# Performance work log

Hardware: AMD Instinct MI355X
Metric: run time of the kernel (lower is better)

The kernel has to match this reference:

```python
import jax, jax.numpy as jnp
import numpy as np

B, S, DIN = 2, 2048, 1024
H = 16
DK = 1024   # dim_key_query_all
DV = 1024   # dim_value_all
DOUT = 1024
HEAD_SIZE = DK / H  # attention_head_size (float division in source)
LN_EPS = 1e-5


def setup_inputs() -> dict:
    key = jax.random.key(0)
    ks = jax.random.split(key, 12)
    s_in = 1.0 / np.sqrt(DIN)
    s_dv = 1.0 / np.sqrt(DV)
    return {
        "hidden_states": jax.random.normal(ks[0], (B, S, DIN), jnp.float32),
        "Wq": jax.random.uniform(ks[1], (DK, DIN), jnp.float32, -s_in, s_in),
        "Wk": jax.random.uniform(ks[2], (DK, DIN), jnp.float32, -s_in, s_in),
        "Wcb": jax.random.uniform(ks[3], (H, DIN), jnp.float32, -s_in, s_in),
        "Wv": jax.random.uniform(ks[4], (DV, DIN), jnp.float32, -s_in, s_in),
        "bv": jax.random.uniform(ks[5], (DV,), jnp.float32, -s_in, s_in),
        "mixing": 0.2 * jax.random.normal(ks[6], (H, DK), jnp.float32),
        "Wd": jax.random.uniform(ks[7], (DOUT, DV), jnp.float32, -s_dv, s_dv),
        "bd": jax.random.uniform(ks[8], (DOUT,), jnp.float32, -s_dv, s_dv),
        "gamma": jnp.ones((DV,), jnp.float32),
        "beta": jnp.zeros((DV,), jnp.float32),
    }


def reference(hidden_states, Wq, Wk, Wcb, Wv, bv, mixing, Wd, bd, gamma, beta):
    x = hidden_states  # [B, S, DIN]; self-attention: from == to
    q = jnp.einsum('bsd,kd->bsk', x, Wq)  # [B,S,DK]
    k = jnp.einsum('bsd,kd->bsk', x, Wk)  # [B,S,DK]
    # scores[b,h,i,j] = sum_c q[b,i,c]*mixing[h,c]*k[b,j,c]
    scores = jnp.einsum('bic,hc,bjc->bhij', q, mixing, k)
    cb = jnp.einsum('bjd,hd->bhj', x, Wcb)  # content bias [B,H,S]
    scores = scores + cb[:, :, None, :]
    scores = scores / jnp.sqrt(jnp.asarray(HEAD_SIZE, scores.dtype))
    probs = jax.nn.softmax(scores, axis=-1)  # dropout p=0.0 -> identity
    v = jnp.einsum('bsd,vd->bsv', x, Wv) + bv  # [B,S,DV]
    v = v.reshape(B, S, H, DV // H)
    ctx = jnp.einsum('bhij,bjhv->bihv', probs, v).reshape(B, S, DV)
    out = jnp.einsum('bsv,ov->bso', ctx, Wd) + bd
    res = x + out
    mu = jnp.mean(res, axis=-1, keepdims=True)
    var = jnp.var(res, axis=-1, keepdims=True)
    out = (res - mu) * jax.lax.rsqrt(var + LN_EPS) * gamma + beta
    return (out,)
```

## Files before the change

kernel.cpp:

```cpp
#include <hip/hip_runtime.h>
#include <cstddef>
#include <cstdint>

#define B_    2
#define S_    2048
#define DIN_  1024
#define H_    16
#define DK_   1024
#define DV_   1024
#define DH_   64
#define DOUT_ 1024
#define M_    (B_ * S_)

typedef __attribute__((ext_vector_type(8)))  short short8;
typedef __attribute__((ext_vector_type(4)))  float float4v;
typedef __attribute__((ext_vector_type(16))) float float16v;
typedef _Float16 half8v __attribute__((ext_vector_type(8)));

__device__ __forceinline__ float bf16s_to_f(short s) {
  union { unsigned int u; float f; } cv;
  cv.u = ((unsigned int)(unsigned short)s) << 16;
  return cv.f;
}
__device__ __forceinline__ short f_to_bf16s(float f) {
  union { float f; unsigned int u; } cv;
  cv.f = f;
  unsigned int u = cv.u + 0x7FFFu + ((cv.u >> 16) & 1u);
  return (short)(u >> 16);
}
__device__ __forceinline__ short f_to_f16s(float f) {
  union { _Float16 h; short s; } cv;
  cv.h = (_Float16)f;
  return cv.s;
}
__device__ __forceinline__ unsigned pkrtz_u32(float a, float b) {
  union { __fp16 __attribute__((ext_vector_type(2))) h2; unsigned u; } cv;
  cv.h2 = __builtin_amdgcn_cvt_pkrtz(a, b);
  return cv.u;
}
__device__ __forceinline__ void gll16(const void* g, void* l) {
  __builtin_amdgcn_global_load_lds(
      (const __attribute__((address_space(1))) unsigned int*)g,
      (__attribute__((address_space(3))) unsigned int*)l, 16, 0, 0);
}

__global__ __launch_bounds__(256) void cast_kernel(const float* __restrict__ in,
                                                   short* __restrict__ out, int n4) {
  int i = blockIdx.x * 256 + threadIdx.x;
  if (i >= n4) return;
  float4 v = ((const float4*)in)[i];
  union { ushort4 u; short s[4]; } o;
  o.s[0] = f_to_bf16s(v.x); o.s[1] = f_to_bf16s(v.y);
  o.s[2] = f_to_bf16s(v.z); o.s[3] = f_to_bf16s(v.w);
  ((ushort4*)out)[i] = o.u;
}

__global__ __launch_bounds__(256) void cb_kernel(const float* __restrict__ x,
                                                 const float* __restrict__ Wcb,
                                                 float* __restrict__ CBs) {
  __shared__ float xs[DIN_];
  const int row = blockIdx.x;
  const int tid = threadIdx.x;
  #pragma unroll
  for (int it = 0; it < 4; ++it)
    xs[tid + it * 256] = x[(size_t)row * DIN_ + tid + it * 256];
  __syncthreads();
  const int lane = tid & 63, w = tid >> 6;
  const float SC = 0.125f * 1.44269504088896f;
  #pragma unroll
  for (int hh = 0; hh < 4; ++hh) {
    const int hidx = w * 4 + hh;
    float p = 0.f;
    for (int c = lane; c < DIN_; c += 64)
      p += xs[c] * Wcb[(size_t)hidx * DIN_ + c];
    #pragma unroll
    for (int mk = 1; mk < 64; mk <<= 1) p += __shfl_xor(p, mk);
    if (lane == 0) {
      const int bb = row / S_, ss = row % S_;
      CBs[((size_t)bb * H_ + hidx) * S_ + ss] = p * SC;
    }
  }
}

__global__ __launch_bounds__(256, 4) void gemm_nt(
    const short* __restrict__ A, const short* __restrict__ Bw,
    const float* __restrict__ bias, const float* __restrict__ resid,
    short* __restrict__ outb, float* __restrict__ outf, int mode) {
  const int KD = 1024, ND = 1024;
  __shared__ __align__(16) short As[64 * 128];
  __shared__ __align__(16) short Bs[64 * 128];
  const int tid  = threadIdx.x;
  const int lane = tid & 63;
  const int w    = tid >> 6;
  const int quad = lane >> 4;
  const int l16  = lane & 15;
  const int m0   = blockIdx.y * 64;
  const int n0   = blockIdx.x * 64;
  const int wm   = (w >> 1) * 32;
  const int wn   = (w & 1) * 32;

  const int drow = lane >> 4;
  const int dp   = lane & 15;

  const float4v zero = {0.f, 0.f, 0.f, 0.f};
  float4v acc[2][2];
  acc[0][0] = zero; acc[0][1] = zero; acc[1][0] = zero; acc[1][1] = zero;

  for (int k0 = 0; k0 < KD; k0 += 128) {
    __syncthreads();
    #pragma unroll
    for (int cc = 0; cc < 4; ++cc) {
      const int n = w * 4 + cc;
      const int r = 4 * n + drow;
      const int l = dp ^ (r & 15);
      gll16(A  + (size_t)(m0 + r) * KD + k0 + l * 8, &As[n * 512]);
      gll16(Bw + (size_t)(n0 + r) * KD + k0 + l * 8, &Bs[n * 512]);
    }
    __syncthreads();
    #pragma unroll
    for (int ks = 0; ks < 4; ++ks) {
      const int ca = ((ks * 4 + quad) ^ l16) * 8;
      short8 af0 = *(short8*)&As[(wm + l16) * 128 + ca];
      short8 af1 = *(short8*)&As[(wm + 16 + l16) * 128 + ca];
      short8 bg0 = *(short8*)&Bs[(wn + l16) * 128 + ca];
      short8 bg1 = *(short8*)&Bs[(wn + 16 + l16) * 128 + ca];
      acc[0][0] = __builtin_amdgcn_mfma_f32_16x16x32_bf16(af0, bg0, acc[0][0], 0, 0, 0);
      acc[0][1] = __builtin_amdgcn_mfma_f32_16x16x32_bf16(af0, bg1, acc[0][1], 0, 0, 0);
      acc[1][0] = __builtin_amdgcn_mfma_f32_16x16x32_bf16(af1, bg0, acc[1][0], 0, 0, 0);
      acc[1][1] = __builtin_amdgcn_mfma_f32_16x16x32_bf16(af1, bg1, acc[1][1], 0, 0, 0);
    }
  }

  #pragma unroll
  for (int mt = 0; mt < 2; ++mt)
    #pragma unroll
    for (int nt = 0; nt < 2; ++nt)
      #pragma unroll
      for (int r = 0; r < 4; ++r) {
        int row = m0 + wm + mt * 16 + quad * 4 + r;
        int col = n0 + wn + nt * 16 + l16;
        float v = acc[mt][nt][r];
        if (mode == 1 || mode == 5) v += bias[col];
        if (mode == 2)
          outf[(size_t)row * ND + col] = v + bias[col] + resid[(size_t)row * ND + col];
        else if (mode == 5) {
          int bb = row >> 11, ss = row & 2047;
          outb[((size_t)bb * DV_ + col) * S_ + ss] = f_to_f16s(v);
        } else if (mode == 4)
          outb[(size_t)row * ND + col] = f_to_f16s(v);
        else
          outb[(size_t)row * ND + col] = f_to_bf16s(v);
      }
}

__global__ __launch_bounds__(256, 2) void attn_kernel(
    const short* __restrict__ Qf, const short* __restrict__ Kf,
    const short* __restrict__ Vtf, const float* __restrict__ mixing,
    const float* __restrict__ CBs, short* __restrict__ ctxb) {
  __shared__ __align__(16) short KsF[2 * 128 * 64];
  __shared__ __align__(16) short Vt[64][136];
  __shared__ __align__(16) short mix_s[DK_];
  __shared__ float cb_s[128];

  const int tid  = threadIdx.x;
  const int lane = tid & 63;
  const int l32  = lane & 31;
  const int l1   = lane >> 5;
  const int w    = tid >> 6;

  const int F    = blockIdx.x;
  const int xcd  = F & 7, rest = F >> 3;
  const int b    = xcd >> 2;
  const int h    = (xcd & 3) * 4 + (rest & 3);
  const int i0   = (rest >> 2) * 128;

  const float SC = 0.125f * 1.44269504088896f;
  for (int c = tid; c < DK_; c += 256) {
    union { _Float16 h; short s; } cv;
    cv.h = (_Float16)(mixing[(size_t)h * DK_ + c] * SC);
    mix_s[c] = cv.s;
  }

  const int iq = i0 + w * 32 + l32;
  const short* qptr  = Qf + ((size_t)b * S_ + iq) * DK_;
  const short* kbase = Kf + (size_t)b * S_ * DK_;
  const short* vtb   = Vtf + ((size_t)b * DV_ + h * DH_) * S_;
  const float* cbp   = CBs + ((size_t)b * H_ + h) * S_;

  float16v accS[4], accO[2];
  #pragma unroll
  for (int g = 0; g < 2; ++g)
    #pragma unroll
    for (int r = 0; r < 16; ++r) accO[g][r] = 0.f;
  float m_run = -1e30f, l_run = 0.f;

  const int nrow = lane >> 3;
  const int dp8  = lane & 7;

  const int vrow = tid >> 2;
  const int vseg = (tid & 3) * 32;

  for (int j0 = 0; j0 < S_; j0 += 128) {
    short8 vreg[4];
    #pragma unroll
    for (int c = 0; c < 4; ++c)
      vreg[c] = *(const short8*)(vtb + (size_t)vrow * S_ + j0 + vseg + c * 8);
    float cbv = 0.f;
    if (tid < 128) cbv = cbp[j0 + tid];
    __syncthreads();
    #pragma unroll
    for (int c = 0; c < 4; ++c)
      *(short8*)&Vt[vrow][vseg + c * 8] = vreg[c];
    if (tid < 128) cb_s[tid] = cbv;

    #pragma unroll
    for (int cc = 0; cc < 4; ++cc) {
      const int n = w * 4 + cc;
      const int r = 8 * n + nrow;
      const int lchunk = dp8 ^ (r & 7);
      gll16(kbase + (size_t)(j0 + r) * DK_ + lchunk * 8, &KsF[n * 512]);
    }
    half8v qcur[4], qnext[4];
    #pragma unroll
    for (int ks = 0; ks < 4; ++ks) {
      qcur[ks] = *(const half8v*)(qptr + ks * 16 + l1 * 8);
      qnext[ks] = qcur[ks];
    }

    #pragma unroll
    for (int f = 0; f < 4; ++f)
      #pragma unroll
      for (int r = 0; r < 16; ++r) accS[f][r] = 0.f;

    __syncthreads();

    for (int t = 0; t < 16; ++t) {
      if (t < 15) {
        const int nb = (t + 1) & 1;
        #pragma unroll
        for (int cc = 0; cc < 4; ++cc) {
          const int n = w * 4 + cc;
          const int r = 8 * n + nrow;
          const int lchunk = dp8 ^ (r & 7);
          gll16(kbase + (size_t)(j0 + r) * DK_ + (t + 1) * 64 + lchunk * 8,
                &KsF[nb * 8192 + n * 512]);
        }
        #pragma unroll
        for (int ks = 0; ks < 4; ++ks)
          qnext[ks] = *(const half8v*)(qptr + (t + 1) * 64 + ks * 16 + l1 * 8);
      }
      const short* kb = &KsF[(t & 1) * 8192];
      __builtin_amdgcn_s_setprio(1);
      #pragma unroll
      for (int ks = 0; ks < 4; ++ks) {
        half8v mf = *(half8v*)&mix_s[t * 64 + ks * 16 + l1 * 8];
        half8v qm = qcur[ks] * mf;
        const int poff = (((2 * ks + l1) ^ (l32 & 7)) * 8) + l32 * 64;
        #pragma unroll
        for (int f = 0; f < 4; ++f) {
          half8v af = *(half8v*)&kb[f * 2048 + poff];
          accS[f] = __builtin_amdgcn_mfma_f32_32x32x16_f16(af, qm, accS[f], 0, 0, 0);
        }
      }
      __builtin_amdgcn_s_setprio(0);
      #pragma unroll
      for (int ks = 0; ks < 4; ++ks) qcur[ks] = qnext[ks];
      __syncthreads();
    }

    float tmax = -1e30f;
    #pragma unroll
    for (int f = 0; f < 4; ++f)
      #pragma unroll
      for (int q = 0; q < 4; ++q) {
        float4 cbq = *(float4*)&cb_s[f * 32 + q * 8 + l1 * 4];
        #pragma unroll
        for (int c = 0; c < 4; ++c) {
          accS[f][4 * q + c] += ((const float*)&cbq)[c];
          tmax = fmaxf(tmax, accS[f][4 * q + c]);
        }
      }
    tmax = fmaxf(tmax, __shfl_xor(tmax, 32));
    const float mnew = fmaxf(m_run, tmax);
    const float alpha = exp2f(m_run - mnew);
    float tsum = 0.f;
    #pragma unroll
    for (int f = 0; f < 4; ++f)
      #pragma unroll
      for (int r = 0; r < 16; ++r) {
        float pv = exp2f(accS[f][r] - mnew);
        accS[f][r] = pv;
        tsum += pv;
      }
    tsum += __shfl_xor(tsum, 32);
    l_run = l_run * alpha + tsum;
    m_run = mnew;
    #pragma unroll
    for (int g = 0; g < 2; ++g)
      #pragma unroll
      for (int r = 0; r < 16; ++r) accO[g][r] *= alpha;

    #pragma unroll
    for (int cpv = 0; cpv < 8; ++cpv) {
      const int t = cpv & 1, fp = cpv >> 1;
      float xo[4], yo[4], lo[4], hi[4];
      #pragma unroll
      for (int c = 0; c < 4; ++c) {
        xo[c] = __shfl_xor(accS[fp][8 * t + c], 32);
        yo[c] = __shfl_xor(accS[fp][8 * t + 4 + c], 32);
      }
      #pragma unroll
      for (int c = 0; c < 4; ++c) {
        lo[c] = l1 ? yo[c] : accS[fp][8 * t + c];
        hi[c] = l1 ? accS[fp][8 * t + 4 + c] : xo[c];
      }
      union { half8v v; unsigned u[4]; } pb;
      pb.u[0] = pkrtz_u32(lo[0], lo[1]);
      pb.u[1] = pkrtz_u32(lo[2], lo[3]);
      pb.u[2] = pkrtz_u32(hi[0], hi[1]);
      pb.u[3] = pkrtz_u32(hi[2], hi[3]);
      #pragma unroll
      for (int g = 0; g < 2; ++g) {
        half8v vf = *(half8v*)&Vt[g * 32 + l32][cpv * 16 + l1 * 8];
        accO[g] = __builtin_amdgcn_mfma_f32_32x32x16_f16(vf, pb.v, accO[g], 0, 0, 0);
      }
    }
  }

  const float rl = 1.0f / l_run;
  short* cbase = ctxb + ((size_t)b * S_ + iq) * DV_ + h * DH_;
  #pragma unroll
  for (int g = 0; g < 2; ++g)
    #pragma unroll
    for (int q = 0; q < 4; ++q) {
      const int dv = g * 32 + 8 * q + 4 * l1;
      union { ushort4 u4; short s[4]; } ov;
      #pragma unroll
      for (int r = 0; r < 4; ++r)
        ov.s[r] = f_to_bf16s(accO[g][4 * q + r] * rl);
      *(ushort4*)(cbase + dv) = ov.u4;
    }
}

__global__ __launch_bounds__(256) void ln_kernel(float* __restrict__ out,
                                                 const float* __restrict__ gamma,
                                                 const float* __restrict__ beta) {
  __shared__ float red[8];
  const int row = blockIdx.x;
  const int tid = threadIdx.x;
  float* p = out + (size_t)row * DOUT_;
  float4 v = ((const float4*)p)[tid];
  float s = v.x + v.y + v.z + v.w;
  #pragma unroll
  for (int mk = 1; mk < 64; mk <<= 1) s += __shfl_xor(s, mk);
  if ((tid & 63) == 0) red[tid >> 6] = s;
  __syncthreads();
  const float mean = (red[0] + red[1] + red[2] + red[3]) * (1.0f / 1024.0f);
  const float d0 = v.x - mean, d1 = v.y - mean, d2 = v.z - mean, d3 = v.w - mean;
  float sq = d0 * d0 + d1 * d1 + d2 * d2 + d3 * d3;
  #pragma unroll
  for (int mk = 1; mk < 64; mk <<= 1) sq += __shfl_xor(sq, mk);
  if ((tid & 63) == 0) red[4 + (tid >> 6)] = sq;
  __syncthreads();
  const float var = (red[4] + red[5] + red[6] + red[7]) * (1.0f / 1024.0f);
  const float rstd = rsqrtf(var + 1e-5f);
  float4 g = ((const float4*)gamma)[tid];
  float4 bt = ((const float4*)beta)[tid];
  float4 o;
  o.x = d0 * rstd * g.x + bt.x;
  o.y = d1 * rstd * g.y + bt.y;
  o.z = d2 * rstd * g.z + bt.z;
  o.w = d3 * rstd * g.w + bt.w;
  ((float4*)p)[tid] = o;
}

extern "C" void kernel_launch(void* const* d_in, const int* in_sizes, int n_in,
                              void* d_out, int out_size, void* d_ws, size_t ws_size,
                              hipStream_t stream) {
  (void)in_sizes; (void)n_in; (void)out_size; (void)ws_size;
  const float* x      = (const float*)d_in[0];
  const float* Wq     = (const float*)d_in[1];
  const float* Wk     = (const float*)d_in[2];
  const float* Wcb    = (const float*)d_in[3];
  const float* Wv     = (const float*)d_in[4];
  const float* bv     = (const float*)d_in[5];
  const float* mixing = (const float*)d_in[6];
  const float* Wd     = (const float*)d_in[7];
  const float* bd     = (const float*)d_in[8];
  const float* gamma  = (const float*)d_in[9];
  const float* beta   = (const float*)d_in[10];
  float* out = (float*)d_out;

  short* p = (short*)d_ws;
  short* xb   = p; p += (size_t)M_ * DIN_;
  short* Qf   = p; p += (size_t)M_ * DK_;
  short* Kf   = p; p += (size_t)M_ * DK_;
  short* Vtf  = p; p += (size_t)B_ * DV_ * S_;
  short* ctxb = p; p += (size_t)M_ * DV_;
  short* Wqb  = p; p += (size_t)DK_ * DIN_;
  short* Wkb  = p; p += (size_t)DK_ * DIN_;
  short* Wvb  = p; p += (size_t)DV_ * DIN_;
  short* Wdb  = p; p += (size_t)DOUT_ * DV_;
  float* CBs  = (float*)p;

  cast_kernel<<<dim3(M_ * DIN_ / 1024), 256, 0, stream>>>(x, xb, M_ * DIN_ / 4);
  cast_kernel<<<dim3(DK_ * DIN_ / 1024), 256, 0, stream>>>(Wq, Wqb, DK_ * DIN_ / 4);
  cast_kernel<<<dim3(DK_ * DIN_ / 1024), 256, 0, stream>>>(Wk, Wkb, DK_ * DIN_ / 4);
  cast_kernel<<<dim3(DV_ * DIN_ / 1024), 256, 0, stream>>>(Wv, Wvb, DV_ * DIN_ / 4);
  cast_kernel<<<dim3(DOUT_ * DV_ / 1024), 256, 0, stream>>>(Wd, Wdb, DOUT_ * DV_ / 4);
  cb_kernel<<<dim3(M_), 256, 0, stream>>>(x, Wcb, CBs);

  dim3 gg(DOUT_ / 64, M_ / 64);
  gemm_nt<<<gg, 256, 0, stream>>>(xb, Wqb, nullptr, nullptr, Qf, nullptr, 4);
  gemm_nt<<<gg, 256, 0, stream>>>(xb, Wkb, nullptr, nullptr, Kf, nullptr, 4);
  gemm_nt<<<gg, 256, 0, stream>>>(xb, Wvb, bv, nullptr, Vtf, nullptr, 5);

  attn_kernel<<<dim3(512), 256, 0, stream>>>(Qf, Kf, Vtf, mixing, CBs, ctxb);

  gemm_nt<<<gg, 256, 0, stream>>>(ctxb, Wdb, bd, x, nullptr, out, 2);
  ln_kernel<<<dim3(M_), 256, 0, stream>>>(out, gamma, beta);
}
```

Measured before the change: 632.3 us.

## Split attention warps into 2x2 query-by-key tiles with split-softmax merge

```diff
diff --git a/kernel.cpp b/kernel.cpp
--- a/kernel.cpp
+++ b/kernel.cpp
@@ -161,12 +161,15 @@
   __shared__ __align__(16) short Vt[64][136];
   __shared__ __align__(16) short mix_s[DK_];
   __shared__ float cb_s[128];
+  __shared__ float mlx[2][2][2][32];
 
   const int tid  = threadIdx.x;
   const int lane = tid & 63;
   const int l32  = lane & 31;
   const int l1   = lane >> 5;
   const int w    = tid >> 6;
+  const int jp   = w & 1;
+  const int qp   = w >> 1;
 
   const int F    = blockIdx.x;
   const int xcd  = F & 7, rest = F >> 3;
@@ -176,23 +179,25 @@
 
   const float SC = 0.125f * 1.44269504088896f;
   for (int c = tid; c < DK_; c += 256) {
-    union { _Float16 h; short s; } cv;
-    cv.h = (_Float16)(mixing[(size_t)h * DK_ + c] * SC);
+    union { _Float16 hh; short s; } cv;
+    cv.hh = (_Float16)(mixing[(size_t)h * DK_ + c] * SC);
     mix_s[c] = cv.s;
   }
 
-  const int iq = i0 + w * 32 + l32;
-  const short* qptr  = Qf + ((size_t)b * S_ + iq) * DK_;
+  const short* qptrA = Qf + ((size_t)b * S_ + i0 + (qp * 2 + 0) * 32 + l32) * DK_;
+  const short* qptrB = Qf + ((size_t)b * S_ + i0 + (qp * 2 + 1) * 32 + l32) * DK_;
   const short* kbase = Kf + (size_t)b * S_ * DK_;
   const short* vtb   = Vtf + ((size_t)b * DV_ + h * DH_) * S_;
   const float* cbp   = CBs + ((size_t)b * H_ + h) * S_;
 
-  float16v accS[4], accO[2];
-  #pragma unroll
-  for (int g = 0; g < 2; ++g)
-    #pragma unroll
-    for (int r = 0; r < 16; ++r) accO[g][r] = 0.f;
-  float m_run = -1e30f, l_run = 0.f;
+  float16v accS[2][2], accO[2][2];
+  #pragma unroll
+  for (int a = 0; a < 2; ++a)
+    #pragma unroll
+    for (int g = 0; g < 2; ++g)
+      #pragma unroll
+      for (int r = 0; r < 16; ++r) accO[a][g][r] = 0.f;
+  float m_run[2] = {-1e30f, -1e30f}, l_run[2] = {0.f, 0.f};
 
   const int nrow = lane >> 3;
   const int dp8  = lane & 7;
@@ -220,17 +225,14 @@
       const int lchunk = dp8 ^ (r & 7);
       gll16(kbase + (size_t)(j0 + r) * DK_ + lchunk * 8, &KsF[n * 512]);
     }
-    half8v qcur[4], qnext[4];
-    #pragma unroll
-    for (int ks = 0; ks < 4; ++ks) {
-      qcur[ks] = *(const half8v*)(qptr + ks * 16 + l1 * 8);
-      qnext[ks] = qcur[ks];
-    }
-
-    #pragma unroll
-    for (int f = 0; f < 4; ++f)
-      #pragma unroll
-      for (int r = 0; r < 16; ++r) accS[f][r] = 0.f;
+
+    float16v accS[2][2];
+    #pragma unroll
+    for (int js = 0; js < 2; ++js)
+      #pragma unroll
+      for (int qs = 0; qs < 2; ++qs)
+        #pragma unroll
+        for (int r = 0; r < 16; ++r) accS[js][qs][r] = 0.f;
 
     __syncthreads();
 
@@ -245,101 +247,136 @@
           gll16(kbase + (size_t)(j0 + r) * DK_ + (t + 1) * 64 + lchunk * 8,
                 &KsF[nb * 8192 + n * 512]);
         }
-        #pragma unroll
-        for (int ks = 0; ks < 4; ++ks)
-          qnext[ks] = *(const half8v*)(qptr + (t + 1) * 64 + ks * 16 + l1 * 8);
+      }
+      half8v qm0[4], qm1[4];
+      #pragma unroll
+      for (int ks = 0; ks < 4; ++ks) {
+        half8v mf = *(half8v*)&mix_s[t * 64 + ks * 16 + l1 * 8];
+        qm0[ks] = *(const half8v*)(qptrA + t * 64 + ks * 16 + l1 * 8) * mf;
+        qm1[ks] = *(const half8v*)(qptrB + t * 64 + ks * 16 + l1 * 8) * mf;
       }
       const short* kb = &KsF[(t & 1) * 8192];
       __builtin_amdgcn_s_setprio(1);
       #pragma unroll
       for (int ks = 0; ks < 4; ++ks) {
-        half8v mf = *(half8v*)&mix_s[t * 64 + ks * 16 + l1 * 8];
-        half8v qm = qcur[ks] * mf;
         const int poff = (((2 * ks + l1) ^ (l32 & 7)) * 8) + l32 * 64;
-        #pragma unroll
-        for (int f = 0; f < 4; ++f) {
-          half8v af = *(half8v*)&kb[f * 2048 + poff];
-          accS[f] = __builtin_amdgcn_mfma_f32_32x32x16_f16(af, qm, accS[f], 0, 0, 0);
-        }
+        half8v af0 = *(half8v*)&kb[(jp * 2 + 0) * 2048 + poff];
+        half8v af1 = *(half8v*)&kb[(jp * 2 + 1) * 2048 + poff];
+        accS[0][0] = __builtin_amdgcn_mfma_f32_32x32x16_f16(af0, qm0[ks], accS[0][0], 0, 0, 0);
+        accS[0][1] = __builtin_amdgcn_mfma_f32_32x32x16_f16(af0, qm1[ks], accS[0][1], 0, 0, 0);
+        accS[1][0] = __builtin_amdgcn_mfma_f32_32x32x16_f16(af1, qm0[ks], accS[1][0], 0, 0, 0);
+        accS[1][1] = __builtin_amdgcn_mfma_f32_32x32x16_f16(af1, qm1[ks], accS[1][1], 0, 0, 0);
       }
       __builtin_amdgcn_s_setprio(0);
-      #pragma unroll
-      for (int ks = 0; ks < 4; ++ks) qcur[ks] = qnext[ks];
       __syncthreads();
     }
 
-    float tmax = -1e30f;
-    #pragma unroll
-    for (int f = 0; f < 4; ++f)
-      #pragma unroll
-      for (int q = 0; q < 4; ++q) {
-        float4 cbq = *(float4*)&cb_s[f * 32 + q * 8 + l1 * 4];
+    #pragma unroll
+    for (int qs = 0; qs < 2; ++qs) {
+      float tmax = -1e30f;
+      #pragma unroll
+      for (int js = 0; js < 2; ++js)
+        #pragma unroll
+        for (int q = 0; q < 4; ++q) {
+          float4 cbq = *(float4*)&cb_s[(jp * 2 + js) * 32 + q * 8 + l1 * 4];
+          #pragma unroll
+          for (int c = 0; c < 4; ++c) {
+            accS[js][qs][4 * q + c] += ((const float*)&cbq)[c];
+            tmax = fmaxf(tmax, accS[js][qs][4 * q + c]);
+          }
+        }
+      tmax = fmaxf(tmax, __shfl_xor(tmax, 32));
+      const float mnew = fmaxf(m_run[qs], tmax);
+      const float alpha = exp2f(m_run[qs] - mnew);
+      float tsum = 0.f;
+      #pragma unroll
+      for (int js = 0; js < 2; ++js)
+        #pragma unroll
+        for (int r = 0; r < 16; ++r) {
+          float pv = exp2f(accS[js][qs][r] - mnew);
+          accS[js][qs][r] = pv;
+          tsum += pv;
+        }
+      tsum += __shfl_xor(tsum, 32);
+      l_run[qs] = l_run[qs] * alpha + tsum;
+      m_run[qs] = mnew;
+      #pragma unroll
+      for (int g = 0; g < 2; ++g)
+        #pragma unroll
+        for (int r = 0; r < 16; ++r) accO[qs][g][r] *= alpha;
+
+      #pragma unroll
+      for (int pv4 = 0; pv4 < 4; ++pv4) {
+        const int js = pv4 >> 1, tt = pv4 & 1;
+        float xo[4], yo[4], lo[4], hi[4];
         #pragma unroll
         for (int c = 0; c < 4; ++c) {
-          accS[f][4 * q + c] += ((const float*)&cbq)[c];
-          tmax = fmaxf(tmax, accS[f][4 * q + c]);
-        }
-      }
-    tmax = fmaxf(tmax, __shfl_xor(tmax, 32));
-    const float mnew = fmaxf(m_run, tmax);
-    const float alpha = exp2f(m_run - mnew);
-    float tsum = 0.f;
-    #pragma unroll
-    for (int f = 0; f < 4; ++f)
-      #pragma unroll
-      for (int r = 0; r < 16; ++r) {
-        float pv = exp2f(accS[f][r] - mnew);
-        accS[f][r] = pv;
-        tsum += pv;
-      }
-    tsum += __shfl_xor(tsum, 32);
-    l_run = l_run * alpha + tsum;
-    m_run = mnew;
-    #pragma unroll
-    for (int g = 0; g < 2; ++g)
-      #pragma unroll
-      for (int r = 0; r < 16; ++r) accO[g][r] *= alpha;
-
-    #pragma unroll
-    for (int cpv = 0; cpv < 8; ++cpv) {
-      const int t = cpv & 1, fp = cpv >> 1;
-      float xo[4], yo[4], lo[4], hi[4];
-      #pragma unroll
-      for (int c = 0; c < 4; ++c) {
-        xo[c] = __shfl_xor(accS[fp][8 * t + c], 32);
-        yo[c] = __shfl_xor(accS[fp][8 * t + 4 + c], 32);
-      }
-      #pragma unroll
-      for (int c = 0; c < 4; ++c) {
-        lo[c] = l1 ? yo[c] : accS[fp][8 * t + c];
-        hi[c] = l1 ? accS[fp][8 * t + 4 + c] : xo[c];
-      }
-      union { half8v v; unsigned u[4]; } pb;
-      pb.u[0] = pkrtz_u32(lo[0], lo[1]);
-      pb.u[1] = pkrtz_u32(lo[2], lo[3]);
-      pb.u[2] = pkrtz_u32(hi[0], hi[1]);
-      pb.u[3] = pkrtz_u32(hi[2], hi[3]);
-      #pragma unroll
-      for (int g = 0; g < 2; ++g) {
-        half8v vf = *(half8v*)&Vt[g * 32 + l32][cpv * 16 + l1 * 8];
-        accO[g] = __builtin_amdgcn_mfma_f32_32x32x16_f16(vf, pb.v, accO[g], 0, 0, 0);
-      }
-    }
-  }
-
-  const float rl = 1.0f / l_run;
-  short* cbase = ctxb + ((size_t)b * S_ + iq) * DV_ + h * DH_;
-  #pragma unroll
-  for (int g = 0; g < 2; ++g)
-    #pragma unroll
-    for (int q = 0; q < 4; ++q) {
-      const int dv = g * 32 + 8 * q + 4 * l1;
-      union { ushort4 u4; short s[4]; } ov;
-      #pragma unroll
-      for (int r = 0; r < 4; ++r)
-        ov.s[r] = f_to_bf16s(accO[g][4 * q + r] * rl);
-      *(ushort4*)(cbase + dv) = ov.u4;
-    }
+          xo[c] = __shfl_xor(accS[js][qs][8 * tt + c], 32);
+          yo[c] = __shfl_xor(accS[js][qs][8 * tt + 4 + c], 32);
+        }
+        #pragma unroll
+        for (int c = 0; c < 4; ++c) {
+          lo[c] = l1 ? yo[c] : accS[js][qs][8 * tt + c];
+          hi[c] = l1 ? accS[js][qs][8 * tt + 4 + c] : xo[c];
+        }
+        union { half8v v; unsigned u[4]; } pb;
+        pb.u[0] = pkrtz_u32(lo[0], lo[1]);
+        pb.u[1] = pkrtz_u32(lo[2], lo[3]);
+        pb.u[2] = pkrtz_u32(hi[0], hi[1]);
+        pb.u[3] = pkrtz_u32(hi[2], hi[3]);
+        const int vcol = ((jp * 2 + js) * 2 + tt) * 16 + l1 * 8;
+        #pragma unroll
+        for (int g = 0; g < 2; ++g) {
+          half8v vf = *(half8v*)&Vt[g * 32 + l32][vcol];
+          accO[qs][g] = __builtin_amdgcn_mfma_f32_32x32x16_f16(vf, pb.v, accO[qs][g], 0, 0, 0);
+        }
+      }
+    }
+  }
+
+  float* buf = (float*)KsF + qp * 4096;
+  if (jp == 1) {
+    #pragma unroll
+    for (int qs = 0; qs < 2; ++qs) {
+      if (l1 == 0) {
+        mlx[qp][qs][0][l32] = m_run[qs];
+        mlx[qp][qs][1][l32] = l_run[qs];
+      }
+      #pragma unroll
+      for (int g = 0; g < 2; ++g)
+        #pragma unroll
+        for (int r = 0; r < 16; ++r)
+          buf[((qs * 2 + g) * 16 + r) * 64 + lane] = accO[qs][g][r];
+    }
+  }
+  __syncthreads();
+  if (jp == 0) {
+    #pragma unroll
+    for (int qs = 0; qs < 2; ++qs) {
+      const float m1 = mlx[qp][qs][0][l32];
+      const float l1v = mlx[qp][qs][1][l32];
+      const float mm = fmaxf(m_run[qs], m1);
+      const float e0 = exp2f(m_run[qs] - mm);
+      const float e1 = exp2f(m1 - mm);
+      const float rl = 1.0f / (l_run[qs] * e0 + l1v * e1);
+      const int q = i0 + (qp * 2 + qs) * 32 + l32;
+      short* cbase = ctxb + ((size_t)b * S_ + q) * DV_ + h * DH_;
+      #pragma unroll
+      for (int g = 0; g < 2; ++g)
+        #pragma unroll
+        for (int q4 = 0; q4 < 4; ++q4) {
+          const int dv = g * 32 + 8 * q4 + 4 * l1;
+          union { ushort4 u4; short s[4]; } ov;
+          #pragma unroll
+          for (int r = 0; r < 4; ++r) {
+            const int reg = 4 * q4 + r;
+            const float o1 = buf[((qs * 2 + g) * 16 + reg) * 64 + lane];
+            ov.s[r] = f_to_bf16s((accO[qs][g][reg] * e0 + o1 * e1) * rl);
+          }
+          *(ushort4*)(cbase + dv) = ov.u4;
+        }
+    }
+  }
 }
 
 __global__ __launch_bounds__(256) void ln_kernel(float* __restrict__ out,
```

Measured after the change: 942.8 us. 49.1% more time.
